# Optimization experiments

Measured on AMD Instinct MI355X. Metric: run time of the kernel, lower is better.

The kernel has to match this reference:

```python
import jax, jax.numpy as jnp
import numpy as np

DIM = 128
B, H, W = 2, 256, 256


def conv2d(x, w, b, groups=1):
    # x: [B,C,H,W], w: [O, C//groups, kh, kw] (OIHW)
    y = jax.lax.conv_general_dilated(
        x, w, window_strides=(1, 1), padding='SAME',
        dimension_numbers=('NCHW', 'OIHW', 'NCHW'),
        feature_group_count=groups)
    return y + b[None, :, None, None]


def l2_normalize(x, axis=-1, eps=1e-12):
    # matches torch.nn.functional.normalize (p=2)
    n = jnp.sqrt(jnp.sum(x * x, axis=axis, keepdims=True))
    return x / jnp.maximum(n, eps)


def setup_inputs() -> dict:
    key = jax.random.key(0)
    ks = jax.random.split(key, 14)
    d = DIM
    h = d // 2
    s = 0.05
    return {
        'x': jax.random.normal(ks[0], (B, d, H, W), dtype=jnp.float32),
        'w_qkv': jax.random.normal(ks[1], (3 * d, d, 1, 1), dtype=jnp.float32) * s,
        'b_qkv': jax.random.normal(ks[2], (3 * d,), dtype=jnp.float32) * s,
        'w_q': jax.random.normal(ks[3], (d, 1, 3, 3), dtype=jnp.float32) * s,
        'b_q': jax.random.normal(ks[4], (d,), dtype=jnp.float32) * s,
        'w_k': jax.random.normal(ks[5], (d, 1, 3, 3), dtype=jnp.float32) * s,
        'b_k': jax.random.normal(ks[6], (d,), dtype=jnp.float32) * s,
        'w_v1': jax.random.normal(ks[7], (h, 2, 3, 3), dtype=jnp.float32) * s,  # groups=d/2, 2 in-ch per group
        'b_v1': jax.random.normal(ks[8], (h,), dtype=jnp.float32) * s,
        'w_v2': jax.random.normal(ks[9], (h, 1, 3, 3), dtype=jnp.float32) * s,  # depthwise on d/2
        'b_v2': jax.random.normal(ks[10], (h,), dtype=jnp.float32) * s,
        'temperature': jnp.ones((d, 1, 1), dtype=jnp.float32),
        'w_po': jax.random.normal(ks[11], (d, d, 1, 1), dtype=jnp.float32) * s,
        'b_po': jax.random.normal(ks[12], (d,), dtype=jnp.float32) * s,
    }


def reference(x, w_qkv, b_qkv, w_q, b_q, w_k, b_k, w_v1, b_v1, w_v2, b_v2,
              temperature, w_po, b_po):
    d = x.shape[1]
    h = d // 2
    # 1x1 conv -> qkv, then split
    qkv = conv2d(x, w_qkv, b_qkv)                     # [B,3d,H,W]
    q, k, v = jnp.split(qkv, 3, axis=1)
    # depthwise 3x3 on q, k
    q = conv2d(q, w_q, b_q, groups=d)
    k = conv2d(k, w_k, b_k, groups=d)
    # MDC on v: grouped conv (2->1 per group), depthwise, concat, sigmoid gate
    x1 = conv2d(v, w_v1, b_v1, groups=h)              # [B,d/2,H,W]
    x2 = conv2d(x1, w_v2, b_v2, groups=h)             # [B,d/2,H,W]
    v = jax.nn.sigmoid(v) * jnp.concatenate([x1, x2], axis=1)
    # per-channel row attention: normalize over W, [B,C,H,H] scores
    q1 = l2_normalize(q, axis=-1)
    k1 = l2_normalize(k, axis=-1)
    scores = jnp.einsum('bchw,bcgw->bchg', q1, k1) * temperature[None]  # [B,C,H,H]
    attn = jax.nn.softmax(scores, axis=-1)
    out = jnp.einsum('bchg,bcgw->bchw', attn, v)      # [B,C,H,W]
    return conv2d(out, w_po, b_po)
```

## Files before the change

kernel.cpp:

```cpp
#include <hip/hip_runtime.h>

typedef unsigned short u16;
typedef unsigned int u32;

#define HW 256
#define PIX 65536

#define WS_T1   100663296ull
#define WS_K1   134217728ull
#define WS_VP   167772160ull
#define WS_NEED 201326592ull

typedef __attribute__((ext_vector_type(8))) short s8v;
typedef __attribute__((ext_vector_type(4))) float f4v;

__device__ __forceinline__ float bu2f(u16 u){ union{u32 i; float f;} x; x.i=((u32)u)<<16; return x.f; }
__device__ __forceinline__ u16 f2bu(float f){ union{float f; u32 i;} x; x.f=f; u32 i=x.i; return (u16)((i + 0x7FFFu + ((i>>16)&1u))>>16); }
__device__ __forceinline__ float sigm(float x){ return 1.0f/(1.0f+__expf(-x)); }
__device__ __forceinline__ u16 cvt_el(float v){ return f2bu(v); }
__device__ __forceinline__ u16 cvt_el(u16 v){ return v; }
__device__ __forceinline__ int swz(int r, int c){ return r*256 + (((c>>3) ^ (r&7))<<3) + (c&7); }
__device__ __forceinline__ int vt_el(int w, int gb){
  int q = (w & 15) ^ gb ^ ((w >> 4) & 7);
  return ((w >> 4) << 10) + (gb << 7) + (q << 3);
}

template<typename TIN>
__global__ __launch_bounds__(256) void k_tr(const TIN* __restrict__ in, u16* __restrict__ outT){
  int t = threadIdx.x;
  int b = blockIdx.y;
  int p = blockIdx.x * 64 + (t >> 2);
  int cc = (t & 3) * 32;
  const TIN* ip = in + ((size_t)(b*128 + cc)) * PIX + p;
  u16 vals[32];
  #pragma unroll
  for (int j = 0; j < 32; ++j) vals[j] = cvt_el(ip[(size_t)j * PIX]);
  u16* op = outT + ((size_t)(b * PIX + p)) * 128 + cc;
  u32 w2[16];
  #pragma unroll
  for (int j = 0; j < 16; ++j) w2[j] = (u32)vals[2*j] | ((u32)vals[2*j+1] << 16);
  uint4* o4 = (uint4*)op;
  o4[0] = make_uint4(w2[0], w2[1], w2[2], w2[3]);
  o4[1] = make_uint4(w2[4], w2[5], w2[6], w2[7]);
  o4[2] = make_uint4(w2[8], w2[9], w2[10], w2[11]);
  o4[3] = make_uint4(w2[12], w2[13], w2[14], w2[15]);
}

template<int OC, bool F32>
__global__ __launch_bounds__(256) void k_gemm(const u16* __restrict__ T, const float* __restrict__ Wg,
                                              const float* __restrict__ bias, int O_total,
                                              void* __restrict__ outv){
  __shared__ u16 Wl[OC * 128];
  int t = threadIdx.x;
  int o_base = blockIdx.y * OC;
  for (int i = t; i < OC * 128; i += 256){
    int o = i >> 7, c = i & 127;
    Wl[(o << 7) | (c ^ ((o & 7) << 3))] = f2bu(Wg[(size_t)(o_base + o) * 128 + c]);
  }
  __syncthreads();

  int wv = t >> 6, l = t & 63;
  int lg = l >> 4, lr = l & 15;
  int p_lin0 = blockIdx.x * 256 + wv * 16;
  int b = (blockIdx.x * 256) >> 16;
  int p_in0 = (p_lin0 & 65535) + lr;

  s8v bf[4][4];
  #pragma unroll
  for (int pt = 0; pt < 4; ++pt){
    const u16* bp = T + (((size_t)(p_lin0 + pt*64 + lr)) << 7) + (lg << 3);
    #pragma unroll
    for (int ks = 0; ks < 4; ++ks)
      bf[pt][ks] = *(const s8v*)(bp + ks * 32);
  }

  for (int ot = 0; ot < OC / 16; ++ot){
    f4v acc[4];
    #pragma unroll
    for (int pt = 0; pt < 4; ++pt) acc[pt] = (f4v){0.f,0.f,0.f,0.f};
    int o = (ot << 4) + lr;
    const u16* wl = Wl + (o << 7);
    int sw = (o & 7) << 3;
    #pragma unroll
    for (int ks = 0; ks < 4; ++ks){
      s8v a = *(const s8v*)(wl + ((((ks << 5) + (lg << 3)) ^ sw)));
      #pragma unroll
      for (int pt = 0; pt < 4; ++pt)
        acc[pt] = __builtin_amdgcn_mfma_f32_16x16x32_bf16(a, bf[pt][ks], acc[pt], 0, 0, 0);
    }
    #pragma unroll
    for (int j = 0; j < 4; ++j){
      int o_row = o_base + (ot << 4) + (lg << 2) + j;
      float bv = bias[o_row];
      size_t base = ((size_t)(b * O_total + o_row)) << 16;
      #pragma unroll
      for (int pt = 0; pt < 4; ++pt){
        if (F32){
          ((float*)outv)[base + p_in0 + pt*64] = acc[pt][j] + bv;
        } else {
          ((u16*)outv)[base + p_in0 + pt*64] = f2bu(acc[pt][j] + bv);
        }
      }
    }
  }
}

__global__ __launch_bounds__(256) void k_dwqk2(const u16* __restrict__ qkv,
                                               const float* __restrict__ w_q, const float* __restrict__ b_q,
                                               const float* __restrict__ w_k, const float* __restrict__ b_k,
                                               u16* __restrict__ q1, u16* __restrict__ k1){
  __shared__ u16 ins[18*272];
  int t = threadIdx.x;
  int chunk = blockIdx.x;
  int c = blockIdx.y;
  int which = blockIdx.z & 1, b = blockIdx.z >> 1;
  const u16* in = qkv + ((size_t)(b*384 + which*128 + c)) * PIX;

  #pragma unroll
  for (int i = t; i < 612; i += 256) ((uint4*)ins)[i] = make_uint4(0,0,0,0);
  __syncthreads();
  int r0 = chunk*16 - 1;
  for (int i = t; i < 576; i += 256){
    int j = i >> 5, k = i & 31;
    int r = r0 + j;
    if (r >= 0 && r < HW)
      *(uint4*)(ins + j*272 + 8 + k*8) = *(const uint4*)(in + r*HW + k*8);
  }
  __syncthreads();

  const float* wk = (which ? w_k : w_q) + c*9;
  float K0=wk[0],K1=wk[1],K2=wk[2],K3=wk[3],K4=wk[4],K5=wk[5],K6=wk[6],K7=wk[7],K8=wk[8];
  float bias = (which ? b_k : b_q)[c];

  int wv = t >> 6, l = t & 63;
  int cb = l * 4;
  float wr[3][6];
  auto ldrow = [&](int j, int slot){
    ushort4 m = *(const ushort4*)(ins + j*272 + 8 + cb);
    wr[slot][0] = bu2f(ins[j*272 + 7 + cb]);
    wr[slot][1] = bu2f(m.x); wr[slot][2] = bu2f(m.y);
    wr[slot][3] = bu2f(m.z); wr[slot][4] = bu2f(m.w);
    wr[slot][5] = bu2f(ins[j*272 + 12 + cb]);
  };
  int rb = wv * 4;
  ldrow(rb, 0); ldrow(rb+1, 1);
  u16* outp = (which ? k1 : q1) + ((size_t)(b*128 + c)) * PIX;
  #pragma unroll
  for (int s = 0; s < 4; ++s){
    ldrow(rb + s + 2, (s+2)%3);
    const float* T = wr[s%3];
    const float* M = wr[(s+1)%3];
    const float* Bo = wr[(s+2)%3];
    float o[4]; float ss = 0.f;
    #pragma unroll
    for (int d = 0; d < 4; ++d){
      float a = bias;
      a = fmaf(K0, T[d], a);  a = fmaf(K1, T[d+1], a);  a = fmaf(K2, T[d+2], a);
      a = fmaf(K3, M[d], a);  a = fmaf(K4, M[d+1], a);  a = fmaf(K5, M[d+2], a);
      a = fmaf(K6, Bo[d], a); a = fmaf(K7, Bo[d+1], a); a = fmaf(K8, Bo[d+2], a);
      o[d] = a;
      ss = fmaf(a, a, ss);
    }
    #pragma unroll
    for (int m = 1; m < 64; m <<= 1) ss += __shfl_xor(ss, m, 64);
    float sc = 1.0f / fmaxf(sqrtf(ss), 1e-12f);
    int row = chunk*16 + rb + s;
    ushort4 pk;
    pk.x = f2bu(o[0]*sc); pk.y = f2bu(o[1]*sc); pk.z = f2bu(o[2]*sc); pk.w = f2bu(o[3]*sc);
    *(ushort4*)(outp + row*HW + cb) = pk;
  }
}

#define MDC_LDS (2*36*272*2 + 34*272*4)

__global__ __launch_bounds__(256,1) void k_mdc2(const u16* __restrict__ qkv,
                                                const float* __restrict__ w_v1, const float* __restrict__ b_v1,
                                                const float* __restrict__ w_v2, const float* __restrict__ b_v2,
                                                u16* __restrict__ vp){
  extern __shared__ char sm[];
  u16*   ins = (u16*)sm;
  float* x1s = (float*)(sm + 2*36*272*2);
  int t = threadIdx.x;
  int chunk = blockIdx.x;
  int g = blockIdx.y;
  int b = blockIdx.z;
  const u16* vbase = qkv + ((size_t)(b*384 + 256)) * PIX;

  #pragma unroll
  for (int i = t; i < 2*36*34; i += 256) ((uint4*)ins)[i] = make_uint4(0,0,0,0);
  for (int i = t; i < 34*68; i += 256) ((uint4*)x1s)[i] = make_uint4(0,0,0,0);
  __syncthreads();
  int r0 = chunk*32 - 2;
  #pragma unroll
  for (int ch = 0; ch < 2; ++ch){
    const u16* src = vbase + (size_t)(2*g + ch) * PIX;
    for (int i = t; i < 1152; i += 256){
      int j = i >> 5, k = i & 31;
      int r = r0 + j;
      if (r >= 0 && r < HW)
        *(uint4*)(ins + ch*36*272 + j*272 + 8 + k*8) = *(const uint4*)(src + r*HW + k*8);
    }
  }
  __syncthreads();

  float W1[18];
  #pragma unroll
  for (int i = 0; i < 18; ++i) W1[i] = w_v1[g*18 + i];
  float B1 = b_v1[g];
  int cb = t + 8;
  float win[2][3][3];
  #pragma unroll
  for (int ch = 0; ch < 2; ++ch)
    #pragma unroll
    for (int rr = 0; rr < 2; ++rr)
      #pragma unroll
      for (int k = 0; k < 3; ++k)
        win[ch][rr][k] = bu2f(ins[ch*36*272 + rr*272 + cb - 1 + k]);
  #pragma unroll
  for (int j = 0; j < 34; ++j){
    #pragma unroll
    for (int ch = 0; ch < 2; ++ch)
      #pragma unroll
      for (int k = 0; k < 3; ++k)
        win[ch][(j+2)%3][k] = bu2f(ins[ch*36*272 + (j+2)*272 + cb - 1 + k]);
    float v = B1;
    #pragma unroll
    for (int ch = 0; ch < 2; ++ch)
      #pragma unroll
      for (int i = 0; i < 3; ++i)
        #pragma unroll
        for (int k = 0; k < 3; ++k)
          v = fmaf(W1[ch*9 + i*3 + k], win[ch][(j+i)%3][k], v);
    int gr = chunk*32 - 1 + j;
    if (gr >= 0 && gr < HW) x1s[j*272 + cb] = v;
  }
  __syncthreads();

  float W2[9];
  #pragma unroll
  for (int i = 0; i < 9; ++i) W2[i] = w_v2[g*9 + i];
  float B2 = b_v2[g];
  const u16* vg   = vbase + (size_t)g * PIX;
  const u16* vg64 = vbase + (size_t)(64 + g) * PIX;
  u16* out0 = vp + ((size_t)(b*128 + g)) * PIX;
  u16* out1 = vp + ((size_t)(b*128 + 64 + g)) * PIX;
  float xw[3][3];
  #pragma unroll
  for (int rr = 0; rr < 2; ++rr)
    #pragma unroll
    for (int k = 0; k < 3; ++k)
      xw[rr][k] = x1s[rr*272 + cb - 1 + k];
  #pragma unroll
  for (int h = 0; h < 32; ++h){
    #pragma unroll
    for (int k = 0; k < 3; ++k)
      xw[(h+2)%3][k] = x1s[(h+2)*272 + cb - 1 + k];
    float x2 = B2;
    #pragma unroll
    for (int i = 0; i < 3; ++i)
      #pragma unroll
      for (int k = 0; k < 3; ++k)
        x2 = fmaf(W2[i*3 + k], xw[(h+i)%3][k], x2);
    int gr = chunk*32 + h;
    float g1 = sigm(bu2f(vg[gr*HW + t]));
    float g2 = sigm(bu2f(vg64[gr*HW + t]));
    float x1c = xw[(h+1)%3][1];
    out0[gr*HW + t] = f2bu(g1 * x1c);
    out1[gr*HW + t] = f2bu(g2 * x2);
  }
}

#define AT2_LDS 163840

__global__ __launch_bounds__(512,1) void k_attn2(const u16* __restrict__ q1, const u16* __restrict__ k1,
                                                 const u16* __restrict__ vp, const float* __restrict__ temp,
                                                 u16* __restrict__ out){
  extern __shared__ char smemraw[];
  u16* Qs = (u16*)smemraw;
  u16* Ks = Qs + 32768;
  u16* Ps = Ks + 16384;
  const int t = threadIdx.x;
  const int l = t & 63;
  const int wv = t >> 6;
  const int c15 = l & 15, h = l >> 4;
  const int blk = blockIdx.x;
  const int plane = blk >> 1, hf = blk & 1;
  const u16* qp  = q1 + (size_t)plane * PIX + hf*128*HW;
  const u16* kp  = k1 + (size_t)plane * PIX;
  const u16* vpp = vp + (size_t)plane * PIX;
  u16* op = out + (size_t)plane * PIX + hf*128*HW;
  const float tc = temp[plane & 127];

  #pragma unroll
  for (int i = 0; i < 8; ++i){
    int c = t + i*512; int row = c >> 5, bc = (c & 31) << 3;
    *(uint4*)(Qs + swz(row, bc)) = *(const uint4*)(qp + row*HW + bc);
  }
  #pragma unroll
  for (int i = 0; i < 4; ++i){
    int c = t + i*512; int row = c >> 5, bc = (c & 31) << 3;
    *(uint4*)(Ks + swz(row, bc)) = *(const uint4*)(kp + row*HW + bc);
  }
  __syncthreads();

  const int r_a = wv*16 + c15;
  s8v qa[8];
  #pragma unroll
  for (int ks = 0; ks < 8; ++ks)
    qa[ks] = *(const s8v*)(Qs + swz(r_a, ks*32 + h*8));

  f4v sacc[16];
  #pragma unroll
  for (int i = 0; i < 16; ++i) sacc[i] = (f4v){0.f,0.f,0.f,0.f};

  uint4 pf[4];
  #pragma unroll
  for (int gt = 0; gt < 4; ++gt){
    {
      const u16* src = (gt < 3) ? (kp + (gt+1)*64*HW) : vpp;
      #pragma unroll
      for (int i = 0; i < 4; ++i){
        int c = t + i*512; int row = c >> 5, bc = (c & 31) << 3;
        pf[i] = *(const uint4*)(src + row*HW + bc);
      }
    }
    #pragma unroll
    for (int gi = 0; gi < 4; ++gi){
      f4v acc = sacc[gt*4 + gi];
      #pragma unroll
      for (int ks = 0; ks < 8; ++ks){
        s8v b = *(const s8v*)(Ks + swz(gi*16 + c15, ks*32 + h*8));
        acc = __builtin_amdgcn_mfma_f32_16x16x32_bf16(qa[ks], b, acc, 0, 0, 0);
      }
      sacc[gt*4 + gi] = acc;
    }
    __syncthreads();
    #pragma unroll
    for (int i = 0; i < 4; ++i){
      int c = t + i*512; int row = c >> 5, bc = (c & 31) << 3;
      *(uint4*)(Ks + swz(row, bc)) = pf[i];
    }
    __syncthreads();
  }

  float mj[4] = {-1e30f,-1e30f,-1e30f,-1e30f};
  #pragma unroll
  for (int i = 0; i < 16; ++i)
    #pragma unroll
    for (int j = 0; j < 4; ++j){
      sacc[i][j] *= tc;
      mj[j] = fmaxf(mj[j], sacc[i][j]);
    }
  #pragma unroll
  for (int j = 0; j < 4; ++j){
    mj[j] = fmaxf(mj[j], __shfl_xor(mj[j], 1, 64));
    mj[j] = fmaxf(mj[j], __shfl_xor(mj[j], 2, 64));
    mj[j] = fmaxf(mj[j], __shfl_xor(mj[j], 4, 64));
    mj[j] = fmaxf(mj[j], __shfl_xor(mj[j], 8, 64));
  }
  float sj[4] = {0.f,0.f,0.f,0.f};
  #pragma unroll
  for (int i = 0; i < 16; ++i)
    #pragma unroll
    for (int j = 0; j < 4; ++j){
      float e = __expf(sacc[i][j] - mj[j]);
      sacc[i][j] = e;
      sj[j] += e;
    }
  #pragma unroll
  for (int j = 0; j < 4; ++j){
    sj[j] += __shfl_xor(sj[j], 1, 64);
    sj[j] += __shfl_xor(sj[j], 2, 64);
    sj[j] += __shfl_xor(sj[j], 4, 64);
    sj[j] += __shfl_xor(sj[j], 8, 64);
    sj[j] = 1.0f / sj[j];
  }
  #pragma unroll
  for (int i = 0; i < 16; ++i)
    #pragma unroll
    for (int j = 0; j < 4; ++j)
      Ps[swz(wv*16 + h*4 + j, i*16 + c15)] = f2bu(sacc[i][j] * sj[j]);
  __syncthreads();

  f4v oacc[16];
  #pragma unroll
  for (int i = 0; i < 16; ++i) oacc[i] = (f4v){0.f,0.f,0.f,0.f};

  #pragma unroll
  for (int gt = 0; gt < 4; ++gt){
    if (gt < 3){
      #pragma unroll
      for (int i = 0; i < 4; ++i){
        int c = t + i*512; int row = c >> 5, bc = (c & 31) << 3;
        pf[i] = *(const uint4*)(vpp + (gt+1)*64*HW + row*HW + bc);
      }
    }
    if (t < 256){
      int gb = t >> 5, wb = t & 31;
      u32 rr[8][4];
      #pragma unroll
      for (int i = 0; i < 8; ++i){
        uint4 v = *(const uint4*)(Ks + (gb*8 + i)*256 + ((wb ^ i) << 3));
        rr[i][0] = v.x; rr[i][1] = v.y; rr[i][2] = v.z; rr[i][3] = v.w;
      }
      #pragma unroll
      for (int j = 0; j < 8; ++j){
        u32 sel = (j & 1) ? 0x07060302u : 0x05040100u;
        int jh = j >> 1;
        u32 o0 = __builtin_amdgcn_perm(rr[1][jh], rr[0][jh], sel);
        u32 o1 = __builtin_amdgcn_perm(rr[3][jh], rr[2][jh], sel);
        u32 o2 = __builtin_amdgcn_perm(rr[5][jh], rr[4][jh], sel);
        u32 o3 = __builtin_amdgcn_perm(rr[7][jh], rr[6][jh], sel);
        int w = wb*8 + j;
        *(uint4*)(Qs + vt_el(w, gb)) = make_uint4(o0, o1, o2, o3);
      }
    }
    __syncthreads();
    if (gt < 3){
      #pragma unroll
      for (int i = 0; i < 4; ++i){
        int c = t + i*512; int row = c >> 5, bc = (c & 31) << 3;
        *(uint4*)(Ks + swz(row, bc)) = pf[i];
      }
    }
    s8v pa[2];
    #pragma unroll
    for (int k2 = 0; k2 < 2; ++k2)
      pa[k2] = *(const s8v*)(Ps + swz(r_a, gt*64 + k2*32 + h*8));
    #pragma unroll
    for (int wt = 0; wt < 16; ++wt){
      f4v acc = oacc[wt];
      #pragma unroll
      for (int k2 = 0; k2 < 2; ++k2){
        int w = wt*16 + c15;
        s8v b = *(const s8v*)(Qs + vt_el(w, (k2 << 2) + h));
        acc = __builtin_amdgcn_mfma_f32_16x16x32_bf16(pa[k2], b, acc, 0, 0, 0);
      }
      oacc[wt] = acc;
    }
    __syncthreads();
  }

  #pragma unroll
  for (int wt = 0; wt < 16; ++wt)
    #pragma unroll
    for (int j = 0; j < 4; ++j)
      Qs[swz(wv*16 + h*4 + j, wt*16 + c15)] = f2bu(oacc[wt][j]);
  __syncthreads();
  #pragma unroll
  for (int i = 0; i < 8; ++i){
    int row = wv*16 + i*2 + (l >> 5);
    int bc = (l & 31) << 3;
    uint4 v = *(const uint4*)(Qs + swz(row, bc));
    *(uint4*)(op + row*HW + bc) = v;
  }
}

extern "C" void kernel_launch(void* const* d_in, const int* in_sizes, int n_in,
                              void* d_out, int out_size, void* d_ws, size_t ws_size,
                              hipStream_t stream){
  (void)in_sizes; (void)n_in; (void)out_size;
  if (ws_size < (size_t)WS_NEED) return;

  const float* x     = (const float*)d_in[0];
  const float* w_qkv = (const float*)d_in[1];
  const float* b_qkv = (const float*)d_in[2];
  const float* w_q   = (const float*)d_in[3];
  const float* b_q   = (const float*)d_in[4];
  const float* w_k   = (const float*)d_in[5];
  const float* b_k   = (const float*)d_in[6];
  const float* w_v1  = (const float*)d_in[7];
  const float* b_v1  = (const float*)d_in[8];
  const float* w_v2  = (const float*)d_in[9];
  const float* b_v2  = (const float*)d_in[10];
  const float* temp  = (const float*)d_in[11];
  const float* w_po  = (const float*)d_in[12];
  const float* b_po  = (const float*)d_in[13];

  char* ws = (char*)d_ws;
  u16*  qkv = (u16*)ws;
  u16*  xT  = (u16*)(ws + WS_T1);
  u16*  q1  = (u16*)(ws + WS_T1);
  u16*  k1  = (u16*)(ws + WS_K1);
  u16*  vp  = (u16*)(ws + WS_VP);
  u16*  aout = qkv;
  u16*  aT  = (u16*)(ws + WS_T1);
  float* out = (float*)d_out;

  k_tr<float><<<dim3(1024, 2), 256, 0, stream>>>(x, xT);
  k_gemm<192, false><<<dim3(512, 2), 256, 0, stream>>>(xT, w_qkv, b_qkv, 384, (void*)qkv);
  k_dwqk2<<<dim3(16, 128, 4), 256, 0, stream>>>(qkv, w_q, b_q, w_k, b_k, q1, k1);
  (void)hipFuncSetAttribute((const void*)k_mdc2, hipFuncAttributeMaxDynamicSharedMemorySize, MDC_LDS);
  k_mdc2<<<dim3(8, 64, 2), 256, MDC_LDS, stream>>>(qkv, w_v1, b_v1, w_v2, b_v2, vp);
  (void)hipFuncSetAttribute((const void*)k_attn2, hipFuncAttributeMaxDynamicSharedMemorySize, AT2_LDS);
  k_attn2<<<512, 512, AT2_LDS, stream>>>(q1, k1, vp, temp, aout);
  k_tr<u16><<<dim3(1024, 2), 256, 0, stream>>>(aout, aT);
  k_gemm<128, true><<<dim3(512, 1), 256, 0, stream>>>(aT, w_po, b_po, 128, (void*)out);
}
```

Measured before the change: 276.8 us.

## Fuse channel transpose into 1x1-conv GEMMs via LDS staging

Removes the separate transpose kernels that wrote pixel-major bf16 copies of the input and attention output to global memory. Each GEMM block now reads its 256-pixel slice of the NCHW tensor directly, converts and transposes it into swizzled LDS, and computes all output channels from there. This saves a full write and read of two large intermediate buffers plus two launches. In exchange, each block holds the whole weight matrix in a large dynamic LDS allocation, limiting occupancy to one block per CU and halving the qkv GEMM grid.

```diff
diff --git a/kernel.cpp b/kernel.cpp
--- a/kernel.cpp
+++ b/kernel.cpp
@@ -20,58 +20,50 @@
 __device__ __forceinline__ u16 cvt_el(float v){ return f2bu(v); }
 __device__ __forceinline__ u16 cvt_el(u16 v){ return v; }
 __device__ __forceinline__ int swz(int r, int c){ return r*256 + (((c>>3) ^ (r&7))<<3) + (c&7); }
+__device__ __forceinline__ int pswz(int p, int c){ return (p<<7) + (((c>>3) ^ (p&7))<<3) + (c&7); }
 __device__ __forceinline__ int vt_el(int w, int gb){
   int q = (w & 15) ^ gb ^ ((w >> 4) & 7);
   return ((w >> 4) << 10) + (gb << 7) + (q << 3);
 }
 
-template<typename TIN>
-__global__ __launch_bounds__(256) void k_tr(const TIN* __restrict__ in, u16* __restrict__ outT){
+template<int OC, typename TIN, bool F32>
+__global__ __launch_bounds__(256,1) void k_gemmP(const TIN* __restrict__ in, const float* __restrict__ Wg,
+                                                 const float* __restrict__ bias, int O_total,
+                                                 void* __restrict__ outv){
+  extern __shared__ u16 lds[];
+  u16* Wl = lds;
+  u16* Xl = lds + OC*128;
   int t = threadIdx.x;
-  int b = blockIdx.y;
-  int p = blockIdx.x * 64 + (t >> 2);
-  int cc = (t & 3) * 32;
-  const TIN* ip = in + ((size_t)(b*128 + cc)) * PIX + p;
-  u16 vals[32];
-  #pragma unroll
-  for (int j = 0; j < 32; ++j) vals[j] = cvt_el(ip[(size_t)j * PIX]);
-  u16* op = outT + ((size_t)(b * PIX + p)) * 128 + cc;
-  u32 w2[16];
-  #pragma unroll
-  for (int j = 0; j < 16; ++j) w2[j] = (u32)vals[2*j] | ((u32)vals[2*j+1] << 16);
-  uint4* o4 = (uint4*)op;
-  o4[0] = make_uint4(w2[0], w2[1], w2[2], w2[3]);
-  o4[1] = make_uint4(w2[4], w2[5], w2[6], w2[7]);
-  o4[2] = make_uint4(w2[8], w2[9], w2[10], w2[11]);
-  o4[3] = make_uint4(w2[12], w2[13], w2[14], w2[15]);
-}
-
-template<int OC, bool F32>
-__global__ __launch_bounds__(256) void k_gemm(const u16* __restrict__ T, const float* __restrict__ Wg,
-                                              const float* __restrict__ bias, int O_total,
-                                              void* __restrict__ outv){
-  __shared__ u16 Wl[OC * 128];
-  int t = threadIdx.x;
-  int o_base = blockIdx.y * OC;
-  for (int i = t; i < OC * 128; i += 256){
+  for (int i = t; i < OC*128; i += 256){
     int o = i >> 7, c = i & 127;
-    Wl[(o << 7) | (c ^ ((o & 7) << 3))] = f2bu(Wg[(size_t)(o_base + o) * 128 + c]);
+    Wl[(o << 7) | (c ^ ((o & 7) << 3))] = f2bu(Wg[(size_t)o*128 + c]);
+  }
+  int p_blk = blockIdx.x * 256;
+  int b = p_blk >> 16;
+  int p0 = p_blk & 65535;
+  {
+    const TIN* col = in + (size_t)b*128*PIX + p0 + t;
+    #pragma unroll 8
+    for (int c2 = 0; c2 < 64; ++c2){
+      int c = c2 * 2;
+      u16 v0 = cvt_el(col[(size_t)c*PIX]);
+      u16 v1 = cvt_el(col[(size_t)(c+1)*PIX]);
+      *(u32*)(Xl + pswz(t, c)) = (u32)v0 | ((u32)v1 << 16);
+    }
   }
   __syncthreads();
 
   int wv = t >> 6, l = t & 63;
   int lg = l >> 4, lr = l & 15;
-  int p_lin0 = blockIdx.x * 256 + wv * 16;
-  int b = (blockIdx.x * 256) >> 16;
-  int p_in0 = (p_lin0 & 65535) + lr;
+  int p_in0 = p0 + wv*16 + lr;
 
   s8v bf[4][4];
   #pragma unroll
   for (int pt = 0; pt < 4; ++pt){
-    const u16* bp = T + (((size_t)(p_lin0 + pt*64 + lr)) << 7) + (lg << 3);
+    int p = wv*16 + pt*64 + lr;
     #pragma unroll
     for (int ks = 0; ks < 4; ++ks)
-      bf[pt][ks] = *(const s8v*)(bp + ks * 32);
+      bf[pt][ks] = *(const s8v*)(Xl + pswz(p, ks*32 + lg*8));
   }
 
   for (int ot = 0; ot < OC / 16; ++ot){
@@ -90,7 +82,7 @@
     }
     #pragma unroll
     for (int j = 0; j < 4; ++j){
-      int o_row = o_base + (ot << 4) + (lg << 2) + j;
+      int o_row = (ot << 4) + (lg << 2) + j;
       float bv = bias[o_row];
       size_t base = ((size_t)(b * O_total + o_row)) << 16;
       #pragma unroll
@@ -104,6 +96,8 @@
     }
   }
 }
+#define GP384_LDS ((384*128 + 256*128) * 2)
+#define GP128_LDS ((128*128 + 256*128) * 2)
 
 __global__ __launch_bounds__(256) void k_dwqk2(const u16* __restrict__ qkv,
                                                const float* __restrict__ w_q, const float* __restrict__ b_q,
@@ -479,21 +473,20 @@
 
   char* ws = (char*)d_ws;
   u16*  qkv = (u16*)ws;
-  u16*  xT  = (u16*)(ws + WS_T1);
   u16*  q1  = (u16*)(ws + WS_T1);
   u16*  k1  = (u16*)(ws + WS_K1);
   u16*  vp  = (u16*)(ws + WS_VP);
   u16*  aout = qkv;
-  u16*  aT  = (u16*)(ws + WS_T1);
   float* out = (float*)d_out;
 
-  k_tr<float><<<dim3(1024, 2), 256, 0, stream>>>(x, xT);
-  k_gemm<192, false><<<dim3(512, 2), 256, 0, stream>>>(xT, w_qkv, b_qkv, 384, (void*)qkv);
+  (void)hipFuncSetAttribute((const void*)k_gemmP<384, float, false>, hipFuncAttributeMaxDynamicSharedMemorySize, GP384_LDS);
+  (void)hipFuncSetAttribute((const void*)k_gemmP<128, u16, true>,   hipFuncAttributeMaxDynamicSharedMemorySize, GP128_LDS);
+
+  k_gemmP<384, float, false><<<512, 256, GP384_LDS, stream>>>(x, w_qkv, b_qkv, 384, (void*)qkv);
   k_dwqk2<<<dim3(16, 128, 4), 256, 0, stream>>>(qkv, w_q, b_q, w_k, b_k, q1, k1);
   (void)hipFuncSetAttribute((const void*)k_mdc2, hipFuncAttributeMaxDynamicSharedMemorySize, MDC_LDS);
   k_mdc2<<<dim3(8, 64, 2), 256, MDC_LDS, stream>>>(qkv, w_v1, b_v1, w_v2, b_v2, vp);
   (void)hipFuncSetAttribute((const void*)k_attn2, hipFuncAttributeMaxDynamicSharedMemorySize, AT2_LDS);
   k_attn2<<<512, 512, AT2_LDS, stream>>>(q1, k1, vp, temp, aout);
-  k_tr<u16><<<dim3(1024, 2), 256, 0, stream>>>(aout, aT);
-  k_gemm<128, true><<<dim3(512, 1), 256, 0, stream>>>(aT, w_po, b_po, 128, (void*)out);
-}
+  k_gemmP<128, u16, true><<<512, 256, GP128_LDS, stream>>>(aout, w_po, b_po, 128, (void*)out);
+}
```

New measurement: 257.2 us. -7.1%, faster.
